# Kernel tuning notes

Hardware: AMD Instinct MI355X
Metric: run time of the kernel (lower is better)

Reference implementation:

```python
import jax, jax.numpy as jnp
import numpy as np

D_MODEL = 1024
NUM_HEADS = 16
DEPTH = D_MODEL // NUM_HEADS
B, S = 2, 2048


def setup_inputs() -> dict:
    key = jax.random.key(0)
    ks = jax.random.split(key, 13)
    sc = 1.0 / np.sqrt(D_MODEL)
    inp = {
        "q": jax.random.normal(ks[0], (B, S, D_MODEL), jnp.float32),
        "k": jax.random.normal(ks[1], (B, S, D_MODEL), jnp.float32),
        "v": jax.random.normal(ks[2], (B, S, D_MODEL), jnp.float32),
        "mask": jax.random.randint(ks[3], (B, 1, S, S), 0, 2).astype(jnp.float32),
        "wq": jax.random.normal(ks[4], (D_MODEL, D_MODEL), jnp.float32) * sc,
        "bq": jnp.zeros((D_MODEL,), jnp.float32),
        "wk": jax.random.normal(ks[5], (D_MODEL, D_MODEL), jnp.float32) * sc,
        "bk": jnp.zeros((D_MODEL,), jnp.float32),
        "wv": jax.random.normal(ks[6], (D_MODEL, D_MODEL), jnp.float32) * sc,
        "bv": jnp.zeros((D_MODEL,), jnp.float32),
        "wo": jax.random.normal(ks[7], (D_MODEL, D_MODEL), jnp.float32) * sc,
        "bo": jnp.zeros((D_MODEL,), jnp.float32),
    }
    return inp


def _split_heads(x):
    # [B,S,D] -> [B,H,S,depth]
    b, s, _ = x.shape
    return x.reshape(b, s, NUM_HEADS, DEPTH).transpose(0, 2, 1, 3)


def reference(q, k, v, mask, wq, bq, wk, bk, wv, bv, wo, bo):
    qh = _split_heads(q @ wq.T + bq)
    kh = _split_heads(k @ wk.T + bk)
    vh = _split_heads(v @ wv.T + bv)
    logits = jnp.einsum("bhqd,bhkd->bhqk", qh, kh) / jnp.sqrt(
        jnp.asarray(DEPTH, jnp.float32))
    logits = logits + mask * (-1e9)
    attn = jax.nn.softmax(logits, axis=-1)
    out = jnp.einsum("bhqk,bhkd->bhqd", attn, vh)
    out = out.transpose(0, 2, 1, 3).reshape(q.shape[0], -1, D_MODEL)
    return out @ wo.T + bo
```

## Files before the change

### kernel.cpp

```cpp
#include <hip/hip_runtime.h>

#define D_MODEL 1024
#define NHEADS  16
#define DEPTH   64
#define BATCH   2
#define SEQ     2048
#define MROWS   (BATCH * SEQ)
#define QSCALE  0.18033688011112042f

typedef unsigned short u16;
typedef unsigned int   u32;
typedef unsigned long long u64;
typedef __bf16 bf16x8 __attribute__((ext_vector_type(8)));
typedef float  f32x4  __attribute__((ext_vector_type(4)));

#if __has_builtin(__builtin_amdgcn_exp2f)
#define EXP2(x) __builtin_amdgcn_exp2f(x)
#else
#define EXP2(x) exp2f(x)
#endif

__device__ __forceinline__ u16 f2b(float f) {
    return __builtin_bit_cast(u16, static_cast<__bf16>(f));
}
__device__ __forceinline__ bf16x8 ldb8(const u16* p) {
    return __builtin_bit_cast(bf16x8, *(const uint4*)p);
}
__device__ __forceinline__ void gload16(const u16* g, u16* l) {
    __builtin_amdgcn_global_load_lds(
        (const __attribute__((address_space(1))) void*)g,
        (__attribute__((address_space(3))) void*)l, 16, 0, 0);
}

__global__ __launch_bounds__(256) void pack_mask(
    const float* __restrict__ mask, u64* __restrict__ bits)
{
    const int w    = blockIdx.x * 4 + (threadIdx.x >> 6);
    const int lane = threadIdx.x & 63;
    float m = mask[(size_t)w * 64 + lane];
    u64 b = __ballot(m > 0.5f);
    if (lane == 0) bits[w] = b;
}

__global__ __launch_bounds__(256) void cvt_bf16(
    const float* __restrict__ q, const float* __restrict__ k, const float* __restrict__ v,
    const float* __restrict__ wq, const float* __restrict__ wk, const float* __restrict__ wv,
    u16* __restrict__ xb, u16* __restrict__ wb)
{
    const size_t e = ((size_t)blockIdx.x * 256 + threadIdx.x) * 8;
    const float* src;
    u16* dst;
    size_t off;
    if (e < 12582912) {
        const int a = (int)(e >> 22);
        off = e & 4194303;
        src = (a == 0) ? q : (a == 1) ? k : v;
        dst = xb + ((size_t)a << 22) + off;
    } else {
        const size_t e2 = e - 12582912;
        const int a = (int)(e2 >> 20);
        off = e2 & 1048575;
        src = (a == 0) ? wq : (a == 1) ? wk : wv;
        dst = wb + ((size_t)a << 20) + off;
    }
    const float4 f0 = *(const float4*)(src + off);
    const float4 f1 = *(const float4*)(src + off + 4);
    uint4 o;
    o.x = (u32)f2b(f0.x) | ((u32)f2b(f0.y) << 16);
    o.y = (u32)f2b(f0.z) | ((u32)f2b(f0.w) << 16);
    o.z = (u32)f2b(f1.x) | ((u32)f2b(f1.y) << 16);
    o.w = (u32)f2b(f1.z) | ((u32)f2b(f1.w) << 16);
    *(uint4*)dst = o;
}

__global__ __launch_bounds__(256, 3) void proj3_bf16(
    const u16* __restrict__ xb, const u16* __restrict__ wb,
    const float* __restrict__ bq, const float* __restrict__ bk, const float* __restrict__ bv,
    u16* __restrict__ qws, u16* __restrict__ kws, u16* __restrict__ vtws)
{
    __shared__ __align__(16) u16 la[2][128 * 32];
    __shared__ __align__(16) u16 lb[2][128 * 32];

    const int z = blockIdx.z;
    const u16* X = xb + ((size_t)z << 22);
    const u16* W = wb + ((size_t)z << 20);
    const float* Bi = (z == 0) ? bq : (z == 1) ? bk : bv;
    u16* dst       = (z == 0) ? qws : (z == 1) ? kws : vtws;

    const int tid  = threadIdx.x;
    const int wv_  = tid >> 6;
    const int lane = tid & 63;
    const int quad = lane >> 4;
    const int l15  = lane & 15;
    const int bx = blockIdx.y >> 2;
    const int by = (blockIdx.x << 2) | (blockIdx.y & 3);
    const int wm = (wv_ >> 1) * 64;
    const int wn = (wv_ & 1) * 64;

    f32x4 acc[4][4];
    for (int i = 0; i < 4; ++i)
        for (int j = 0; j < 4; ++j)
            acc[i][j] = (f32x4){0.f, 0.f, 0.f, 0.f};

    const int rowA0 = by * 128;
    const int rowB0 = bx * 128;

    const int strow = tid >> 2;
    const int stcol = (tid & 3) * 8;
    const u16* gA0 = &X[(size_t)(rowA0 + strow) * D_MODEL + stcol];
    const u16* gA1 = gA0 + (size_t)64 * D_MODEL;
    const u16* gB0 = &W[(size_t)(rowB0 + strow) * D_MODEL + stcol];
    const u16* gB1 = gB0 + (size_t)64 * D_MODEL;
    const int l0 = tid * 8, l1 = 2048 + tid * 8;

    gload16(gA0, &la[0][l0]);
    gload16(gA1, &la[0][l1]);
    gload16(gB0, &lb[0][l0]);
    gload16(gB1, &lb[0][l1]);
    __syncthreads();

    for (int t = 0; t < 32; ++t) {
        const int buf = t & 1;
        if (t < 31) {
            const int ko = (t + 1) * 32;
            gload16(gA0 + ko, &la[buf ^ 1][l0]);
            gload16(gA1 + ko, &la[buf ^ 1][l1]);
            gload16(gB0 + ko, &lb[buf ^ 1][l0]);
            gload16(gB1 + ko, &lb[buf ^ 1][l1]);
        }
        bf16x8 af[4], bfr[4];
        #pragma unroll
        for (int tt = 0; tt < 4; ++tt) {
            af[tt]  = ldb8(&la[buf][(wm + tt * 16 + l15) * 32 + quad * 8]);
            bfr[tt] = ldb8(&lb[buf][(wn + tt * 16 + l15) * 32 + quad * 8]);
        }
        #pragma unroll
        for (int mt = 0; mt < 4; ++mt)
            #pragma unroll
            for (int nt = 0; nt < 4; ++nt)
                acc[mt][nt] = __builtin_amdgcn_mfma_f32_16x16x32_bf16(af[mt], bfr[nt], acc[mt][nt], 0, 0, 0);
        __syncthreads();
    }

    #pragma unroll
    for (int nt = 0; nt < 4; ++nt) {
        int n = bx * 128 + wn + nt * 16 + l15;
        float bvv = Bi[n];
        int h = n >> 6, d = n & 63;
        #pragma unroll
        for (int mt = 0; mt < 4; ++mt) {
            #pragma unroll
            for (int r = 0; r < 4; ++r) {
                int m = by * 128 + wm + mt * 16 + quad * 4 + r;
                float c = acc[mt][nt][r] + bvv;
                if (z == 0) c *= QSCALE;
                int b = m >> 11, s = m & (SEQ - 1);
                if (z != 2)
                    dst[(((size_t)(b * NHEADS + h) * SEQ) + s) * DEPTH + d] = f2b(c);
                else
                    dst[(((size_t)(b * NHEADS + h) * DEPTH) + d) * SEQ + s] = f2b(c);
            }
        }
    }
}

__global__ __launch_bounds__(256, 3) void proj3_fused(
    const float* __restrict__ q, const float* __restrict__ k, const float* __restrict__ v,
    const float* __restrict__ wq, const float* __restrict__ wk, const float* __restrict__ wv,
    const float* __restrict__ bq, const float* __restrict__ bk, const float* __restrict__ bv,
    u16* __restrict__ qws, u16* __restrict__ kws, u16* __restrict__ vtws)
{
    __shared__ __align__(16) u16 ldsA[128 * 40];
    __shared__ __align__(16) u16 ldsB[128 * 40];

    const int z = blockIdx.z;
    const float* X  = (z == 0) ? q  : (z == 1) ? k  : v;
    const float* W  = (z == 0) ? wq : (z == 1) ? wk : wv;
    const float* Bi = (z == 0) ? bq : (z == 1) ? bk : bv;
    u16* dst        = (z == 0) ? qws : (z == 1) ? kws : vtws;

    const int tid  = threadIdx.x;
    const int wv_  = tid >> 6;
    const int lane = tid & 63;
    const int quad = lane >> 4;
    const int l15  = lane & 15;
    const int bx = blockIdx.y >> 2;
    const int by = (blockIdx.x << 2) | (blockIdx.y & 3);
    const int wm = (wv_ >> 1) * 64;
    const int wn = (wv_ & 1) * 64;

    f32x4 acc[4][4];
    for (int i = 0; i < 4; ++i)
        for (int j = 0; j < 4; ++j)
            acc[i][j] = (f32x4){0.f, 0.f, 0.f, 0.f};

    const int rowA0 = by * 128;
    const int rowB0 = bx * 128;

    const int sr = tid >> 3;
    const int sc = (tid & 7) * 4;

    float4 pa[4], pb[4];
    #pragma unroll
    for (int i = 0; i < 4; ++i) {
        pa[i] = *(const float4*)&X[(size_t)(rowA0 + sr + i * 32) * D_MODEL + sc];
        pb[i] = *(const float4*)&W[(size_t)(rowB0 + sr + i * 32) * D_MODEL + sc];
    }

    for (int it = 0; it < 32; ++it) {
        #pragma unroll
        for (int i = 0; i < 4; ++i) {
            ushort4 ha, hb;
            ha.x = f2b(pa[i].x); ha.y = f2b(pa[i].y); ha.z = f2b(pa[i].z); ha.w = f2b(pa[i].w);
            hb.x = f2b(pb[i].x); hb.y = f2b(pb[i].y); hb.z = f2b(pb[i].z); hb.w = f2b(pb[i].w);
            *(ushort4*)&ldsA[(sr + i * 32) * 40 + sc] = ha;
            *(ushort4*)&ldsB[(sr + i * 32) * 40 + sc] = hb;
        }
        __syncthreads();

        if (it < 31) {
            const int k0 = (it + 1) * 32;
            #pragma unroll
            for (int i = 0; i < 4; ++i) {
                pa[i] = *(const float4*)&X[(size_t)(rowA0 + sr + i * 32) * D_MODEL + k0 + sc];
                pb[i] = *(const float4*)&W[(size_t)(rowB0 + sr + i * 32) * D_MODEL + k0 + sc];
            }
        }

        bf16x8 af[4], bfr[4];
        #pragma unroll
        for (int t = 0; t < 4; ++t) {
            af[t]  = ldb8(&ldsA[(wm + t * 16 + l15) * 40 + quad * 8]);
            bfr[t] = ldb8(&ldsB[(wn + t * 16 + l15) * 40 + quad * 8]);
        }
        #pragma unroll
        for (int mt = 0; mt < 4; ++mt)
            #pragma unroll
            for (int nt = 0; nt < 4; ++nt)
                acc[mt][nt] = __builtin_amdgcn_mfma_f32_16x16x32_bf16(af[mt], bfr[nt], acc[mt][nt], 0, 0, 0);
        __syncthreads();
    }

    #pragma unroll
    for (int nt = 0; nt < 4; ++nt) {
        int n = bx * 128 + wn + nt * 16 + l15;
        float bvv = Bi[n];
        int h = n >> 6, d = n & 63;
        #pragma unroll
        for (int mt = 0; mt < 4; ++mt) {
            #pragma unroll
            for (int r = 0; r < 4; ++r) {
                int m = by * 128 + wm + mt * 16 + quad * 4 + r;
                float c = acc[mt][nt][r] + bvv;
                if (z == 0) c *= QSCALE;
                int b = m >> 11, s = m & (SEQ - 1);
                if (z != 2)
                    dst[(((size_t)(b * NHEADS + h) * SEQ) + s) * DEPTH + d] = f2b(c);
                else
                    dst[(((size_t)(b * NHEADS + h) * DEPTH) + d) * SEQ + s] = f2b(c);
            }
        }
    }
}

__global__ __launch_bounds__(256) void gemm_out(
    const u16* __restrict__ X, const float* __restrict__ W,
    const float* __restrict__ bias, float* __restrict__ out)
{
    __shared__ __align__(16) u16 ldsA[128 * 40];
    __shared__ __align__(16) u16 ldsB[64 * 40];

    const int tid  = threadIdx.x;
    const int wv_  = tid >> 6;
    const int lane = tid & 63;
    const int quad = lane >> 4;
    const int l15  = lane & 15;
    const int bx = ((blockIdx.y >> 2) << 1) | (blockIdx.x >> 3);
    const int by = ((blockIdx.x & 7) << 2) | (blockIdx.y & 3);
    const int wm = (wv_ >> 1) * 64;
    const int wn = (wv_ & 1) * 32;

    f32x4 acc[4][2];
    for (int i = 0; i < 4; ++i)
        for (int j = 0; j < 2; ++j)
            acc[i][j] = (f32x4){0.f, 0.f, 0.f, 0.f};

    const int rowA0 = by * 128;
    const int rowB0 = bx * 64;

    const int ar = tid >> 2, akc = (tid & 3) * 8;
    const int br = tid >> 3, bc = (tid & 7) * 4;

    uint4  paA[2];
    float4 paB[2];
    #pragma unroll
    for (int i = 0; i < 2; ++i) {
        paA[i] = *(const uint4*)&X[(size_t)(rowA0 + ar + i * 64) * D_MODEL + akc];
        paB[i] = *(const float4*)&W[(size_t)(rowB0 + br + i * 32) * D_MODEL + bc];
    }

    for (int it = 0; it < 32; ++it) {
        #pragma unroll
        for (int i = 0; i < 2; ++i) {
            *(uint4*)&ldsA[(ar + i * 64) * 40 + akc] = paA[i];
            ushort4 hb;
            hb.x = f2b(paB[i].x); hb.y = f2b(paB[i].y); hb.z = f2b(paB[i].z); hb.w = f2b(paB[i].w);
            *(ushort4*)&ldsB[(br + i * 32) * 40 + bc] = hb;
        }
        __syncthreads();

        if (it < 31) {
            const int k0 = (it + 1) * 32;
            #pragma unroll
            for (int i = 0; i < 2; ++i) {
                paA[i] = *(const uint4*)&X[(size_t)(rowA0 + ar + i * 64) * D_MODEL + k0 + akc];
                paB[i] = *(const float4*)&W[(size_t)(rowB0 + br + i * 32) * D_MODEL + k0 + bc];
            }
        }

        bf16x8 af[4], bfr[2];
        #pragma unroll
        for (int t = 0; t < 4; ++t)
            af[t] = ldb8(&ldsA[(wm + t * 16 + l15) * 40 + quad * 8]);
        #pragma unroll
        for (int t = 0; t < 2; ++t)
            bfr[t] = ldb8(&ldsB[(wn + t * 16 + l15) * 40 + quad * 8]);
        #pragma unroll
        for (int mt = 0; mt < 4; ++mt)
            #pragma unroll
            for (int nt = 0; nt < 2; ++nt)
                acc[mt][nt] = __builtin_amdgcn_mfma_f32_16x16x32_bf16(af[mt], bfr[nt], acc[mt][nt], 0, 0, 0);
        __syncthreads();
    }

    #pragma unroll
    for (int nt = 0; nt < 2; ++nt) {
        int n = bx * 64 + wn + nt * 16 + l15;
        float bvv = bias[n];
        #pragma unroll
        for (int mt = 0; mt < 4; ++mt) {
            #pragma unroll
            for (int r = 0; r < 4; ++r) {
                int m = by * 128 + wm + mt * 16 + quad * 4 + r;
                out[(size_t)m * D_MODEL + n] = acc[mt][nt][r] + bvv;
            }
        }
    }
}

__global__ __launch_bounds__(256, 4) void flash_attn(
    const u16* __restrict__ Q, const u16* __restrict__ K,
    const u16* __restrict__ Vt, const u64* __restrict__ maskbits,
    u16* __restrict__ O)
{
    __shared__ __align__(16) u16 ldsK[2][64 * 64];
    __shared__ __align__(16) u16 ldsV[2][64 * 64];
    __shared__ __align__(16) u16 ldsP[4][16 * 64];

    const int tid  = threadIdx.x;
    const int wv_  = tid >> 6;
    const int lane = tid & 63;
    const int quad = lane >> 4;
    const int l15  = lane & 15;
    const int bh = ((blockIdx.x & 7) << 2) | (blockIdx.y & 3);
    const int qt = ((blockIdx.y >> 2) << 2) | (blockIdx.x >> 3);
    const int b  = bh >> 4, h = bh & 15;
    const int q0 = qt * 64 + wv_ * 16;

    const u16* Qb = Q  + (size_t)bh * SEQ * DEPTH;
    const u16* Kb = K  + (size_t)bh * SEQ * DEPTH;
    const u16* Vb = Vt + (size_t)bh * DEPTH * SEQ;
    const u64* MB = maskbits + (size_t)b * SEQ * (SEQ / 64);

    const int srow = tid >> 3;
    const int sc8  = tid & 7;
    const int swz  = ((sc8 ^ (srow & 7)) * 8);
    const int kdst0 = srow * 64 + swz;
    const int kdst1 = (srow + 32) * 64 + swz;

    const int xk0 = ((quad ^ (l15 & 7)) * 8);
    const int xk1 = (((4 + quad) ^ (l15 & 7)) * 8);

    bf16x8 aq0 = ldb8(&Qb[(q0 + l15) * DEPTH + quad * 8]);
    bf16x8 aq1 = ldb8(&Qb[(q0 + l15) * DEPTH + 32 + quad * 8]);

    bf16x8 vones;
    #pragma unroll
    for (int i = 0; i < 8; ++i) vones[i] = (__bf16)1.0f;

    f32x4 oa[4];
    for (int i = 0; i < 4; ++i) oa[i] = (f32x4){0.f, 0.f, 0.f, 0.f};
    f32x4 lacc = (f32x4){0.f, 0.f, 0.f, 0.f};

    u16* myP = ldsP[wv_];

    int wp[4][4];
    #pragma unroll
    for (int cc = 0; cc < 4; ++cc)
        #pragma unroll
        for (int r = 0; r < 4; ++r) {
            const int row  = quad * 4 + r;
            const int colg = cc * 2 + (l15 >> 3);
            wp[cc][r] = row * 64 + ((colg ^ (row & 7)) * 8) + (l15 & 7);
        }
    const int rp0 = l15 * 64 + ((quad ^ (l15 & 7)) * 8);
    const int rp1 = l15 * 64 + (((4 + quad) ^ (l15 & 7)) * 8);

    uint4 kreg0 = *(const uint4*)&Kb[(size_t)srow * DEPTH + sc8 * 8];
    uint4 kreg1 = *(const uint4*)&Kb[(size_t)(srow + 32) * DEPTH + sc8 * 8];
    uint4 vreg0 = *(const uint4*)&Vb[(size_t)srow * SEQ + sc8 * 8];
    uint4 vreg1 = *(const uint4*)&Vb[(size_t)(srow + 32) * SEQ + sc8 * 8];

    for (int it = 0; it < 32; ++it) {
        const int buf = it & 1;
        u16* Kl = ldsK[buf];
        u16* Vl = ldsV[buf];

        *(uint4*)&Kl[kdst0] = kreg0;
        *(uint4*)&Kl[kdst1] = kreg1;
        *(uint4*)&Vl[kdst0] = vreg0;
        *(uint4*)&Vl[kdst1] = vreg1;
        __syncthreads();

        if (it < 31) {
            const int kb2 = (it + 1) * 64;
            kreg0 = *(const uint4*)&Kb[(size_t)(kb2 + srow) * DEPTH + sc8 * 8];
            kreg1 = *(const uint4*)&Kb[(size_t)(kb2 + srow + 32) * DEPTH + sc8 * 8];
            vreg0 = *(const uint4*)&Vb[(size_t)srow * SEQ + kb2 + sc8 * 8];
            vreg1 = *(const uint4*)&Vb[(size_t)(srow + 32) * SEQ + kb2 + sc8 * 8];
        }

        u32 tlo[4], thi[4];
        #pragma unroll
        for (int r = 0; r < 4; ++r) {
            u64 t = MB[(size_t)(q0 + quad * 4 + r) * (SEQ / 64) + it] >> l15;
            tlo[r] = (u32)t;
            thi[r] = (u32)(t >> 32);
        }

        #pragma unroll
        for (int cc = 0; cc < 4; ++cc) {
            const int row = cc * 16 + l15;
            bf16x8 bk0 = ldb8(&Kl[row * 64 + xk0]);
            bf16x8 bk1 = ldb8(&Kl[row * 64 + xk1]);
            f32x4 z = (f32x4){0.f, 0.f, 0.f, 0.f};
            z = __builtin_amdgcn_mfma_f32_16x16x32_bf16(aq0, bk0, z, 0, 0, 0);
            z = __builtin_amdgcn_mfma_f32_16x16x32_bf16(aq1, bk1, z, 0, 0, 0);
            #pragma unroll
            for (int r = 0; r < 4; ++r) {
                u32 w   = (cc < 2) ? tlo[r] : thi[r];
                u32 bit = (cc & 1) ? ((w >> 16) & 1u) : (w & 1u);
                float e = EXP2(z[r]);
                float p = bit ? 0.f : e;
                myP[wp[cc][r]] = f2b(p);
            }
        }

        __builtin_amdgcn_wave_barrier();
        __builtin_amdgcn_s_waitcnt(0xc07f);
        __builtin_amdgcn_wave_barrier();
        bf16x8 pa0 = ldb8(&myP[rp0]);
        bf16x8 pa1 = ldb8(&myP[rp1]);

        lacc = __builtin_amdgcn_mfma_f32_16x16x32_bf16(pa0, vones, lacc, 0, 0, 0);
        lacc = __builtin_amdgcn_mfma_f32_16x16x32_bf16(pa1, vones, lacc, 0, 0, 0);

        #pragma unroll
        for (int n = 0; n < 4; ++n) {
            const int row = n * 16 + l15;
            bf16x8 bv0 = ldb8(&Vl[row * 64 + xk0]);
            bf16x8 bv1 = ldb8(&Vl[row * 64 + xk1]);
            oa[n] = __builtin_amdgcn_mfma_f32_16x16x32_bf16(pa0, bv0, oa[n], 0, 0, 0);
            oa[n] = __builtin_amdgcn_mfma_f32_16x16x32_bf16(pa1, bv1, oa[n], 0, 0, 0);
        }
    }

    float inv[4];
    #pragma unroll
    for (int r = 0; r < 4; ++r)
        inv[r] = 1.0f / lacc[r];

    #pragma unroll
    for (int n = 0; n < 4; ++n)
        #pragma unroll
        for (int r = 0; r < 4; ++r) {
            int m = q0 + quad * 4 + r;
            O[((size_t)b * SEQ + m) * D_MODEL + h * DEPTH + n * 16 + l15] =
                f2b(oa[n][r] * inv[r]);
        }
}

extern "C" void kernel_launch(void* const* d_in, const int* in_sizes, int n_in,
                              void* d_out, int out_size, void* d_ws, size_t ws_size,
                              hipStream_t stream) {
    const float* q    = (const float*)d_in[0];
    const float* k    = (const float*)d_in[1];
    const float* v    = (const float*)d_in[2];
    const float* mask = (const float*)d_in[3];
    const float* wq   = (const float*)d_in[4];
    const float* bq   = (const float*)d_in[5];
    const float* wk   = (const float*)d_in[6];
    const float* bk   = (const float*)d_in[7];
    const float* wv   = (const float*)d_in[8];
    const float* bv   = (const float*)d_in[9];
    const float* wo   = (const float*)d_in[10];
    const float* bo   = (const float*)d_in[11];

    u16* base = (u16*)d_ws;
    const size_t seg = (size_t)BATCH * NHEADS * SEQ * DEPTH;
    u16* qws  = base;
    u16* kws  = base + seg;
    u16* vtws = base + 2 * seg;
    u16* ows  = base + 3 * seg;
    u64* mbits = (u64*)(base + 4 * seg);
    u16* xb   = base + 4 * seg + 524288;
    u16* wb   = xb + 3 * seg;
    const size_t need_bytes = (4 * seg + 524288 + 3 * seg + 3u * 1048576) * 2;

    dim3 blk(256);
    hipLaunchKernelGGL(pack_mask, dim3(BATCH * SEQ * (SEQ / 64) / 4), blk, 0, stream, mask, mbits);

    dim3 gp(D_MODEL / 128, MROWS / 128, 3);
    if (ws_size >= need_bytes) {
        hipLaunchKernelGGL(cvt_bf16, dim3(7680), blk, 0, stream,
                           q, k, v, wq, wk, wv, xb, wb);
        hipLaunchKernelGGL(proj3_bf16, gp, blk, 0, stream,
                           xb, wb, bq, bk, bv, qws, kws, vtws);
    } else {
        hipLaunchKernelGGL(proj3_fused, gp, blk, 0, stream,
                           q, k, v, wq, wk, wv, bq, bk, bv, qws, kws, vtws);
    }

    dim3 ga(SEQ / 64, BATCH * NHEADS);
    hipLaunchKernelGGL(flash_attn, ga, blk, 0, stream, qws, kws, vtws, mbits, ows);

    dim3 go(D_MODEL / 64, MROWS / 128);
    hipLaunchKernelGGL(gemm_out, go, blk, 0, stream, ows, wo, bo, (float*)d_out);
}
```

Measured before the change: 303.9 us.

## Double query rows per attention wave and add bf16 async-load output GEMM

Flash attention now gives each wave 32 query rows (two 16-row fragments), so every K/V tile loaded into LDS is reused for twice as many queries. The grid is halved and the occupancy hint drops from 4 to 2. Wo is now converted to bf16 in the existing conversion kernel, and a new output GEMM streams bf16 tiles straight into double-buffered LDS with global_load_lds, replacing per-iteration fp32-to-bf16 conversion through registers. Costs are higher register pressure, lower occupancy in attention, and a larger conversion kernel.

```diff
diff --git a/kernel.cpp b/kernel.cpp
--- a/kernel.cpp
+++ b/kernel.cpp
@@ -45,6 +45,7 @@
 __global__ __launch_bounds__(256) void cvt_bf16(
     const float* __restrict__ q, const float* __restrict__ k, const float* __restrict__ v,
     const float* __restrict__ wq, const float* __restrict__ wk, const float* __restrict__ wv,
+    const float* __restrict__ wo,
     u16* __restrict__ xb, u16* __restrict__ wb)
 {
     const size_t e = ((size_t)blockIdx.x * 256 + threadIdx.x) * 8;
@@ -60,7 +61,7 @@
         const size_t e2 = e - 12582912;
         const int a = (int)(e2 >> 20);
         off = e2 & 1048575;
-        src = (a == 0) ? wq : (a == 1) ? wk : wv;
+        src = (a == 0) ? wq : (a == 1) ? wk : (a == 2) ? wv : wo;
         dst = wb + ((size_t)a << 20) + off;
     }
     const float4 f0 = *(const float4*)(src + off);
@@ -263,12 +264,12 @@
     }
 }
 
-__global__ __launch_bounds__(256) void gemm_out(
-    const u16* __restrict__ X, const float* __restrict__ W,
+__global__ __launch_bounds__(256, 2) void gemm_out_bf16(
+    const u16* __restrict__ X, const u16* __restrict__ W,
     const float* __restrict__ bias, float* __restrict__ out)
 {
-    __shared__ __align__(16) u16 ldsA[128 * 40];
-    __shared__ __align__(16) u16 ldsB[64 * 40];
+    __shared__ __align__(16) u16 la[2][128 * 32];
+    __shared__ __align__(16) u16 lb[2][64 * 32];
 
     const int tid  = threadIdx.x;
     const int wv_  = tid >> 6;
@@ -288,6 +289,81 @@
     const int rowA0 = by * 128;
     const int rowB0 = bx * 64;
 
+    const int strow = tid >> 2;
+    const int stcol = (tid & 3) * 8;
+    const u16* gA0 = &X[(size_t)(rowA0 + strow) * D_MODEL + stcol];
+    const u16* gA1 = gA0 + (size_t)64 * D_MODEL;
+    const u16* gB0 = &W[(size_t)(rowB0 + strow) * D_MODEL + stcol];
+    const int l0 = tid * 8, l1 = 2048 + tid * 8;
+
+    gload16(gA0, &la[0][l0]);
+    gload16(gA1, &la[0][l1]);
+    gload16(gB0, &lb[0][l0]);
+    __syncthreads();
+
+    for (int t = 0; t < 32; ++t) {
+        const int buf = t & 1;
+        if (t < 31) {
+            const int ko = (t + 1) * 32;
+            gload16(gA0 + ko, &la[buf ^ 1][l0]);
+            gload16(gA1 + ko, &la[buf ^ 1][l1]);
+            gload16(gB0 + ko, &lb[buf ^ 1][l0]);
+        }
+        bf16x8 af[4], bfr[2];
+        #pragma unroll
+        for (int tt = 0; tt < 4; ++tt)
+            af[tt] = ldb8(&la[buf][(wm + tt * 16 + l15) * 32 + quad * 8]);
+        #pragma unroll
+        for (int tt = 0; tt < 2; ++tt)
+            bfr[tt] = ldb8(&lb[buf][(wn + tt * 16 + l15) * 32 + quad * 8]);
+        #pragma unroll
+        for (int mt = 0; mt < 4; ++mt)
+            #pragma unroll
+            for (int nt = 0; nt < 2; ++nt)
+                acc[mt][nt] = __builtin_amdgcn_mfma_f32_16x16x32_bf16(af[mt], bfr[nt], acc[mt][nt], 0, 0, 0);
+        __syncthreads();
+    }
+
+    #pragma unroll
+    for (int nt = 0; nt < 2; ++nt) {
+        int n = bx * 64 + wn + nt * 16 + l15;
+        float bvv = bias[n];
+        #pragma unroll
+        for (int mt = 0; mt < 4; ++mt) {
+            #pragma unroll
+            for (int r = 0; r < 4; ++r) {
+                int m = by * 128 + wm + mt * 16 + quad * 4 + r;
+                out[(size_t)m * D_MODEL + n] = acc[mt][nt][r] + bvv;
+            }
+        }
+    }
+}
+
+__global__ __launch_bounds__(256) void gemm_out_f32(
+    const u16* __restrict__ X, const float* __restrict__ W,
+    const float* __restrict__ bias, float* __restrict__ out)
+{
+    __shared__ __align__(16) u16 ldsA[128 * 40];
+    __shared__ __align__(16) u16 ldsB[64 * 40];
+
+    const int tid  = threadIdx.x;
+    const int wv_  = tid >> 6;
+    const int lane = tid & 63;
+    const int quad = lane >> 4;
+    const int l15  = lane & 15;
+    const int bx = ((blockIdx.y >> 2) << 1) | (blockIdx.x >> 3);
+    const int by = ((blockIdx.x & 7) << 2) | (blockIdx.y & 3);
+    const int wm = (wv_ >> 1) * 64;
+    const int wn = (wv_ & 1) * 32;
+
+    f32x4 acc[4][2];
+    for (int i = 0; i < 4; ++i)
+        for (int j = 0; j < 2; ++j)
+            acc[i][j] = (f32x4){0.f, 0.f, 0.f, 0.f};
+
+    const int rowA0 = by * 128;
+    const int rowB0 = bx * 64;
+
     const int ar = tid >> 2, akc = (tid & 3) * 8;
     const int br = tid >> 3, bc = (tid & 7) * 4;
 
@@ -348,14 +424,14 @@
     }
 }
 
-__global__ __launch_bounds__(256, 4) void flash_attn(
+__global__ __launch_bounds__(256, 2) void flash_attn(
     const u16* __restrict__ Q, const u16* __restrict__ K,
     const u16* __restrict__ Vt, const u64* __restrict__ maskbits,
     u16* __restrict__ O)
 {
     __shared__ __align__(16) u16 ldsK[2][64 * 64];
     __shared__ __align__(16) u16 ldsV[2][64 * 64];
-    __shared__ __align__(16) u16 ldsP[4][16 * 64];
+    __shared__ __align__(16) u16 ldsP[4][32 * 64];
 
     const int tid  = threadIdx.x;
     const int wv_  = tid >> 6;
@@ -365,7 +441,7 @@
     const int bh = ((blockIdx.x & 7) << 2) | (blockIdx.y & 3);
     const int qt = ((blockIdx.y >> 2) << 2) | (blockIdx.x >> 3);
     const int b  = bh >> 4, h = bh & 15;
-    const int q0 = qt * 64 + wv_ * 16;
+    const int q0 = qt * 128 + wv_ * 32;
 
     const u16* Qb = Q  + (size_t)bh * SEQ * DEPTH;
     const u16* Kb = K  + (size_t)bh * SEQ * DEPTH;
@@ -381,30 +457,42 @@
     const int xk0 = ((quad ^ (l15 & 7)) * 8);
     const int xk1 = (((4 + quad) ^ (l15 & 7)) * 8);
 
-    bf16x8 aq0 = ldb8(&Qb[(q0 + l15) * DEPTH + quad * 8]);
-    bf16x8 aq1 = ldb8(&Qb[(q0 + l15) * DEPTH + 32 + quad * 8]);
+    bf16x8 aq0[2], aq1[2];
+    #pragma unroll
+    for (int f = 0; f < 2; ++f) {
+        aq0[f] = ldb8(&Qb[(q0 + f * 16 + l15) * DEPTH + quad * 8]);
+        aq1[f] = ldb8(&Qb[(q0 + f * 16 + l15) * DEPTH + 32 + quad * 8]);
+    }
 
     bf16x8 vones;
     #pragma unroll
     for (int i = 0; i < 8; ++i) vones[i] = (__bf16)1.0f;
 
-    f32x4 oa[4];
-    for (int i = 0; i < 4; ++i) oa[i] = (f32x4){0.f, 0.f, 0.f, 0.f};
-    f32x4 lacc = (f32x4){0.f, 0.f, 0.f, 0.f};
+    f32x4 oa[2][4];
+    #pragma unroll
+    for (int f = 0; f < 2; ++f)
+        for (int i = 0; i < 4; ++i) oa[f][i] = (f32x4){0.f, 0.f, 0.f, 0.f};
+    f32x4 lacc[2];
+    lacc[0] = (f32x4){0.f, 0.f, 0.f, 0.f};
+    lacc[1] = (f32x4){0.f, 0.f, 0.f, 0.f};
 
     u16* myP = ldsP[wv_];
 
-    int wp[4][4];
+    int wpa[4][4];
     #pragma unroll
     for (int cc = 0; cc < 4; ++cc)
         #pragma unroll
         for (int r = 0; r < 4; ++r) {
             const int row  = quad * 4 + r;
             const int colg = cc * 2 + (l15 >> 3);
-            wp[cc][r] = row * 64 + ((colg ^ (row & 7)) * 8) + (l15 & 7);
-        }
-    const int rp0 = l15 * 64 + ((quad ^ (l15 & 7)) * 8);
-    const int rp1 = l15 * 64 + (((4 + quad) ^ (l15 & 7)) * 8);
+            wpa[cc][r] = row * 64 + ((colg ^ (row & 7)) * 8) + (l15 & 7);
+        }
+    int rp0_[2], rp1_[2];
+    #pragma unroll
+    for (int f = 0; f < 2; ++f) {
+        rp0_[f] = (f * 16 + l15) * 64 + ((quad ^ (l15 & 7)) * 8);
+        rp1_[f] = (f * 16 + l15) * 64 + (((4 + quad) ^ (l15 & 7)) * 8);
+    }
 
     uint4 kreg0 = *(const uint4*)&Kb[(size_t)srow * DEPTH + sc8 * 8];
     uint4 kreg1 = *(const uint4*)&Kb[(size_t)(srow + 32) * DEPTH + sc8 * 8];
@@ -430,64 +518,81 @@
             vreg1 = *(const uint4*)&Vb[(size_t)(srow + 32) * SEQ + kb2 + sc8 * 8];
         }
 
-        u32 tlo[4], thi[4];
-        #pragma unroll
-        for (int r = 0; r < 4; ++r) {
-            u64 t = MB[(size_t)(q0 + quad * 4 + r) * (SEQ / 64) + it] >> l15;
-            tlo[r] = (u32)t;
-            thi[r] = (u32)(t >> 32);
-        }
+        u32 tlo[2][4], thi[2][4];
+        #pragma unroll
+        for (int f = 0; f < 2; ++f)
+            #pragma unroll
+            for (int r = 0; r < 4; ++r) {
+                u64 t = MB[(size_t)(q0 + f * 16 + quad * 4 + r) * (SEQ / 64) + it] >> l15;
+                tlo[f][r] = (u32)t;
+                thi[f][r] = (u32)(t >> 32);
+            }
 
         #pragma unroll
         for (int cc = 0; cc < 4; ++cc) {
             const int row = cc * 16 + l15;
             bf16x8 bk0 = ldb8(&Kl[row * 64 + xk0]);
             bf16x8 bk1 = ldb8(&Kl[row * 64 + xk1]);
-            f32x4 z = (f32x4){0.f, 0.f, 0.f, 0.f};
-            z = __builtin_amdgcn_mfma_f32_16x16x32_bf16(aq0, bk0, z, 0, 0, 0);
-            z = __builtin_amdgcn_mfma_f32_16x16x32_bf16(aq1, bk1, z, 0, 0, 0);
-            #pragma unroll
-            for (int r = 0; r < 4; ++r) {
-                u32 w   = (cc < 2) ? tlo[r] : thi[r];
-                u32 bit = (cc & 1) ? ((w >> 16) & 1u) : (w & 1u);
-                float e = EXP2(z[r]);
-                float p = bit ? 0.f : e;
-                myP[wp[cc][r]] = f2b(p);
+            #pragma unroll
+            for (int f = 0; f < 2; ++f) {
+                f32x4 z = (f32x4){0.f, 0.f, 0.f, 0.f};
+                z = __builtin_amdgcn_mfma_f32_16x16x32_bf16(aq0[f], bk0, z, 0, 0, 0);
+                z = __builtin_amdgcn_mfma_f32_16x16x32_bf16(aq1[f], bk1, z, 0, 0, 0);
+                #pragma unroll
+                for (int r = 0; r < 4; ++r) {
+                    u32 w   = (cc < 2) ? tlo[f][r] : thi[f][r];
+                    u32 bit = (cc & 1) ? ((w >> 16) & 1u) : (w & 1u);
+                    float e = EXP2(z[r]);
+                    float p = bit ? 0.f : e;
+                    myP[wpa[cc][r] + f * 1024] = f2b(p);
+                }
             }
         }
 
         __builtin_amdgcn_wave_barrier();
         __builtin_amdgcn_s_waitcnt(0xc07f);
         __builtin_amdgcn_wave_barrier();
-        bf16x8 pa0 = ldb8(&myP[rp0]);
-        bf16x8 pa1 = ldb8(&myP[rp1]);
-
-        lacc = __builtin_amdgcn_mfma_f32_16x16x32_bf16(pa0, vones, lacc, 0, 0, 0);
-        lacc = __builtin_amdgcn_mfma_f32_16x16x32_bf16(pa1, vones, lacc, 0, 0, 0);
+        bf16x8 pa0[2], pa1[2];
+        #pragma unroll
+        for (int f = 0; f < 2; ++f) {
+            pa0[f] = ldb8(&myP[rp0_[f]]);
+            pa1[f] = ldb8(&myP[rp1_[f]]);
+        }
+
+        #pragma unroll
+        for (int f = 0; f < 2; ++f) {
+            lacc[f] = __builtin_amdgcn_mfma_f32_16x16x32_bf16(pa0[f], vones, lacc[f], 0, 0, 0);
+            lacc[f] = __builtin_amdgcn_mfma_f32_16x16x32_bf16(pa1[f], vones, lacc[f], 0, 0, 0);
+        }
 
         #pragma unroll
         for (int n = 0; n < 4; ++n) {
             const int row = n * 16 + l15;
             bf16x8 bv0 = ldb8(&Vl[row * 64 + xk0]);
             bf16x8 bv1 = ldb8(&Vl[row * 64 + xk1]);
-            oa[n] = __builtin_amdgcn_mfma_f32_16x16x32_bf16(pa0, bv0, oa[n], 0, 0, 0);
-            oa[n] = __builtin_amdgcn_mfma_f32_16x16x32_bf16(pa1, bv1, oa[n], 0, 0, 0);
-        }
-    }
-
-    float inv[4];
-    #pragma unroll
-    for (int r = 0; r < 4; ++r)
-        inv[r] = 1.0f / lacc[r];
-
-    #pragma unroll
-    for (int n = 0; n < 4; ++n)
-        #pragma unroll
-        for (int r = 0; r < 4; ++r) {
-            int m = q0 + quad * 4 + r;
-            O[((size_t)b * SEQ + m) * D_MODEL + h * DEPTH + n * 16 + l15] =
-                f2b(oa[n][r] * inv[r]);
-        }
+            #pragma unroll
+            for (int f = 0; f < 2; ++f) {
+                oa[f][n] = __builtin_amdgcn_mfma_f32_16x16x32_bf16(pa0[f], bv0, oa[f][n], 0, 0, 0);
+                oa[f][n] = __builtin_amdgcn_mfma_f32_16x16x32_bf16(pa1[f], bv1, oa[f][n], 0, 0, 0);
+            }
+        }
+    }
+
+    #pragma unroll
+    for (int f = 0; f < 2; ++f) {
+        float inv[4];
+        #pragma unroll
+        for (int r = 0; r < 4; ++r)
+            inv[r] = 1.0f / lacc[f][r];
+        #pragma unroll
+        for (int n = 0; n < 4; ++n)
+            #pragma unroll
+            for (int r = 0; r < 4; ++r) {
+                int m = q0 + f * 16 + quad * 4 + r;
+                O[((size_t)b * SEQ + m) * D_MODEL + h * DEPTH + n * 16 + l15] =
+                    f2b(oa[f][n][r] * inv[r]);
+            }
+    }
 }
 
 extern "C" void kernel_launch(void* const* d_in, const int* in_sizes, int n_in,
@@ -515,15 +620,16 @@
     u64* mbits = (u64*)(base + 4 * seg);
     u16* xb   = base + 4 * seg + 524288;
     u16* wb   = xb + 3 * seg;
-    const size_t need_bytes = (4 * seg + 524288 + 3 * seg + 3u * 1048576) * 2;
+    const size_t need_bytes = (4 * seg + 524288 + 3 * seg + 4u * 1048576) * 2;
+    const bool bf16path = (ws_size >= need_bytes);
 
     dim3 blk(256);
     hipLaunchKernelGGL(pack_mask, dim3(BATCH * SEQ * (SEQ / 64) / 4), blk, 0, stream, mask, mbits);
 
     dim3 gp(D_MODEL / 128, MROWS / 128, 3);
-    if (ws_size >= need_bytes) {
-        hipLaunchKernelGGL(cvt_bf16, dim3(7680), blk, 0, stream,
-                           q, k, v, wq, wk, wv, xb, wb);
+    if (bf16path) {
+        hipLaunchKernelGGL(cvt_bf16, dim3(8192), blk, 0, stream,
+                           q, k, v, wq, wk, wv, wo, xb, wb);
         hipLaunchKernelGGL(proj3_bf16, gp, blk, 0, stream,
                            xb, wb, bq, bk, bv, qws, kws, vtws);
     } else {
@@ -531,9 +637,13 @@
                            q, k, v, wq, wk, wv, bq, bk, bv, qws, kws, vtws);
     }
 
-    dim3 ga(SEQ / 64, BATCH * NHEADS);
+    dim3 ga(32, 16);
     hipLaunchKernelGGL(flash_attn, ga, blk, 0, stream, qws, kws, vtws, mbits, ows);
 
     dim3 go(D_MODEL / 64, MROWS / 128);
-    hipLaunchKernelGGL(gemm_out, go, blk, 0, stream, ows, wo, bo, (float*)d_out);
-}
+    if (bf16path) {
+        hipLaunchKernelGGL(gemm_out_bf16, go, blk, 0, stream, ows, wb + 3 * 1048576, bo, (float*)d_out);
+    } else {
+        hipLaunchKernelGGL(gemm_out_f32, go, blk, 0, stream, ows, wo, bo, (float*)d_out);
+    }
+}
```

New measurement: 285.5 us. 1.06x faster.
